# Performance work log

Hardware: AMD Instinct MI355X
Metric: run time of the kernel (lower is better)

The kernel has to match this reference:

```python
import jax, jax.numpy as jnp
import numpy as np

SEQ_LEN = 4_194_304  # number of tokens
INPUT_BITS = 16      # bits per token, MSB first


def setup_inputs() -> dict:
    key = jax.random.key(0)
    # bits in {0,1}; float32 carrier (values exact, matches uint8 bit semantics)
    tokens = jax.random.randint(key, (SEQ_LEN, INPUT_BITS), 0, 2).astype(jnp.float32)
    return {"tokens": tokens}


def reference(tokens):
    # tokens: [seq_len, input_bits], MSB first, entries in {0,1}
    bits = tokens.shape[1]
    # _bits_to_int: val = val*2 + b  ==  dot with [2^(bits-1), ..., 2, 1]
    pow2 = jnp.exp2(jnp.arange(bits - 1, -1, -1, dtype=jnp.float32))  # [bits]
    values = tokens @ pow2  # [seq_len], exact for bits <= 24
    # stable ascending sort == Python list.sort on (value, original_index)
    order = jnp.argsort(values, stable=True)  # [seq_len]
    return tokens[order]  # gather rows by rank
```

## Files before the change

### kernel.cpp

```cpp
#include <hip/hip_runtime.h>
#include <stdint.h>

static constexpr uint32_t SEQN = 4194304u;
static constexpr uint32_t BINS = 65536u;
static constexpr uint32_t QWORDS = BINS / 4u;
static constexpr uint32_t NBLK = 256u;
static constexpr uint32_t NTHR = 1024u;
static constexpr uint32_t ROWS_PER_BLK = SEQN / NBLK;

__global__ __launch_bounds__(NTHR) void k_hist_lds(const float4* __restrict__ in4,
                                                   uint32_t* __restrict__ partial,
                                                   uint32_t* __restrict__ blkTot) {
  __shared__ __align__(16) uint32_t h[QWORDS];
  uint32_t tid = threadIdx.x, blk = blockIdx.x;
  if (blk == 0u && tid < 64u) blkTot[tid] = 0u;
  uint4* hv = (uint4*)h;
  for (uint32_t i = tid; i < QWORDS / 4u; i += NTHR) hv[i] = make_uint4(0u, 0u, 0u, 0u);
  __syncthreads();
  uint32_t q = tid & 3u;
  uint32_t shift = 12u - (q << 2);
  bool leader = (q == 0u);
  const float4* base = in4 + (size_t)blk * (ROWS_PER_BLK * 4u);
#pragma unroll
  for (uint32_t b = 0; b < 8u; ++b) {
    float4 v[8];
#pragma unroll
    for (uint32_t u = 0; u < 8u; ++u)
      v[u] = base[(size_t)(b * 8u + u) * NTHR + tid];
#pragma unroll
    for (uint32_t u = 0; u < 8u; ++u) {
      float nf = ((v[u].x * 2.0f + v[u].y) * 2.0f + v[u].z) * 2.0f + v[u].w;
      uint32_t part = ((uint32_t)nf) << shift;
      uint32_t s1 = part + (uint32_t)__builtin_amdgcn_mov_dpp((int)part, 0xB1, 0xF, 0xF, true);
      uint32_t key = s1 + (uint32_t)__builtin_amdgcn_mov_dpp((int)s1, 0x4E, 0xF, 0xF, true);
      if (leader) atomicAdd(&h[key >> 2], 1u << ((key & 3u) << 3));
    }
  }
  __syncthreads();
  uint4* dst = (uint4*)(partial + (size_t)blk * QWORDS);
  for (uint32_t i = tid; i < QWORDS / 4u; i += NTHR) dst[i] = hv[i];
}

__global__ __launch_bounds__(256) void k_reduceD(const uint32_t* __restrict__ partial,
                                                 uint32_t* __restrict__ hist,
                                                 uint32_t* __restrict__ blkTot) {
  __shared__ uint2 acc[4][64];
  uint32_t tid = threadIdx.x, b = blockIdx.x;
  uint32_t wl = tid & 63u, g = tid >> 6;
  uint32_t w = b * 64u + wl;
  uint32_t e = 0u, o = 0u;
  uint32_t p0 = g * 64u;
#pragma unroll 8
  for (uint32_t p = p0; p < p0 + 64u; ++p) {
    uint32_t v = partial[(size_t)p * QWORDS + w];
    e += v & 0x00FF00FFu;
    o += (v >> 8) & 0x00FF00FFu;
  }
  acc[g][wl] = make_uint2(e, o);
  __syncthreads();
  if (g == 0u) {
    uint2 a1 = acc[1][wl], a2 = acc[2][wl], a3 = acc[3][wl];
    e += a1.x + a2.x + a3.x;
    o += a1.y + a2.y + a3.y;
    uint32_t c0 = e & 0xFFFFu, c2 = e >> 16, c1 = o & 0xFFFFu, c3 = o >> 16;
    ((uint4*)hist)[w] = make_uint4(c0, c1, c2, c3);
    uint32_t ssum = c0 + c1 + c2 + c3;
    for (int d = 1; d < 64; d <<= 1) ssum += __shfl_xor(ssum, d, 64);
    if (wl == 0u) atomicAdd(&blkTot[b >> 2], ssum);
  }
}

__global__ __launch_bounds__(256) void k_zero(uint32_t* __restrict__ hist,
                                              uint32_t* __restrict__ blkTot) {
  uint32_t i = blockIdx.x * 256u + threadIdx.x;
  if (i < BINS) hist[i] = 0u;
  if (i < 64u) blkTot[i] = 0u;
}

__global__ __launch_bounds__(256) void k_hist(const float4* __restrict__ in4,
                                              uint32_t* __restrict__ hist) {
  uint32_t r = blockIdx.x * 256u + threadIdx.x;
  if (r >= SEQN) return;
  uint32_t key = 0u;
#pragma unroll
  for (uint32_t qq = 0; qq < 4u; ++qq) {
    float4 v = in4[(size_t)r * 4u + qq];
    uint32_t nib = ((uint32_t)v.x << 3) | ((uint32_t)v.y << 2) |
                   ((uint32_t)v.z << 1) | (uint32_t)v.w;
    key = (key << 4) | nib;
  }
  atomicAdd(&hist[key], 1u);
}

__global__ __launch_bounds__(256) void k_scan1(const uint32_t* __restrict__ hist,
                                               uint32_t* __restrict__ blkTot) {
  uint32_t tid = threadIdx.x, blk = blockIdx.x;
  uint32_t b0 = blk * 1024u + tid * 4u;
  uint32_t s = hist[b0] + hist[b0 + 1] + hist[b0 + 2] + hist[b0 + 3];
  for (int d = 1; d < 64; d <<= 1) s += __shfl_xor(s, d, 64);
  __shared__ uint32_t wt[4];
  if ((tid & 63u) == 0u) wt[tid >> 6] = s;
  __syncthreads();
  if (tid == 0u) blkTot[blk] = wt[0] + wt[1] + wt[2] + wt[3];
}

__global__ __launch_bounds__(256) void k_scanB(const uint32_t* __restrict__ hist,
                                               const uint32_t* __restrict__ blkTot,
                                               uint32_t* __restrict__ offs) {
  __shared__ uint32_t s_base;
  __shared__ uint32_t wt[4];
  uint32_t tid = threadIdx.x, blk = blockIdx.x;
  if (tid < 64u) {
    uint32_t v = blkTot[tid];
    uint32_t incl = v;
    for (int d = 1; d < 64; d <<= 1) {
      uint32_t n = __shfl_up(incl, d, 64);
      if (tid >= (uint32_t)d) incl += n;
    }
    if (tid == blk) s_base = incl - v;
  }
  __syncthreads();
  uint32_t lane = tid & 63u, wid = tid >> 6;
  uint32_t b0 = blk * 1024u + tid * 4u;
  uint4 c = ((const uint4*)hist)[b0 >> 2];
  uint32_t s = c.x + c.y + c.z + c.w;
  uint32_t incl = s;
  for (int d = 1; d < 64; d <<= 1) {
    uint32_t n = __shfl_up(incl, d, 64);
    if (lane >= (uint32_t)d) incl += n;
  }
  if (lane == 63u) wt[wid] = incl;
  __syncthreads();
  uint32_t wbase = 0u;
  for (uint32_t w = 0; w < wid; ++w) wbase += wt[w];
  uint32_t base = s_base + wbase + (incl - s);
  ((uint4*)offs)[b0 >> 2] = make_uint4(base, base + c.x, base + c.x + c.y,
                                       base + c.x + c.y + c.z);
}

__global__ __launch_bounds__(256) void k_write(const uint32_t* __restrict__ hist,
                                               const uint32_t* __restrict__ offs,
                                               float4* __restrict__ out4) {
  __shared__ uint32_t s_off[32], s_cnt[32];
  uint32_t tid = threadIdx.x, blk = blockIdx.x;
  if (tid < 32u) {
    uint32_t k = blk * 32u + tid;
    s_off[tid] = offs[k];
    s_cnt[tid] = hist[k];
  }
  __syncthreads();
  uint32_t lane = tid & 63u, wid = tid >> 6;
  uint32_t q = lane & 3u;
  for (uint32_t kk = 0; kk < 8u; ++kk) {
    uint32_t ki = wid * 8u + kk;
    uint32_t k = blk * 32u + ki;
    uint32_t off = s_off[ki], cnt = s_cnt[ki];
    float4 pat;
    pat.x = (float)((k >> (15u - (q * 4u + 0u))) & 1u);
    pat.y = (float)((k >> (15u - (q * 4u + 1u))) & 1u);
    pat.z = (float)((k >> (15u - (q * 4u + 2u))) & 1u);
    pat.w = (float)((k >> (15u - (q * 4u + 3u))) & 1u);
    size_t base = (size_t)off * 4u;
    uint32_t tot = cnt * 4u;
    for (uint32_t j = lane; j < tot; j += 64u) out4[base + j] = pat;
  }
}

extern "C" void kernel_launch(void* const* d_in, const int* in_sizes, int n_in,
                              void* d_out, int out_size, void* d_ws, size_t ws_size,
                              hipStream_t stream) {
  const float4* in4 = (const float4*)d_in[0];
  float4* out4 = (float4*)d_out;
  uint32_t* hist = (uint32_t*)d_ws;
  uint32_t* offs = hist + BINS;
  uint32_t* blkTot = offs + BINS;
  uint32_t* partial = blkTot + 1024u;

  size_t need = ((size_t)2 * BINS + 1024u + (size_t)NBLK * QWORDS) * 4u;
  if (ws_size >= need) {
    k_hist_lds<<<NBLK, NTHR, 0, stream>>>(in4, partial, blkTot);
    k_reduceD<<<256, 256, 0, stream>>>(partial, hist, blkTot);
  } else {
    k_zero<<<BINS / 256, 256, 0, stream>>>(hist, blkTot);
    k_hist<<<SEQN / 256, 256, 0, stream>>>(in4, hist);
    k_scan1<<<64, 256, 0, stream>>>(hist, blkTot);
  }
  k_scanB<<<64, 256, 0, stream>>>(hist, blkTot, offs);
  k_write<<<BINS / 32, 256, 0, stream>>>(hist, offs, out4);
}
```

Baseline: 134.2 us.

## Write output by row slabs using binary search over bin offsets

The output writer now maps threads to output rows instead of histogram bins. Each block binary-searches the exclusive prefix offsets to find the key for each of its 2048 rows, stages the keys in LDS, then writes fully coalesced float4 runs. This removes the load imbalance and partial-wavefront stores that came from variable bin counts. The cost is 16 dependent global loads per row for the search, though those reads mostly hit cache.

```diff
diff --git a/kernel.cpp b/kernel.cpp
--- a/kernel.cpp
+++ b/kernel.cpp
@@ -138,31 +138,36 @@
                                        base + c.x + c.y + c.z);
 }
 
-__global__ __launch_bounds__(256) void k_write(const uint32_t* __restrict__ hist,
-                                               const uint32_t* __restrict__ offs,
-                                               float4* __restrict__ out4) {
-  __shared__ uint32_t s_off[32], s_cnt[32];
+__global__ __launch_bounds__(256) void k_write_slab(const uint32_t* __restrict__ offs,
+                                                    float4* __restrict__ out4) {
+  __shared__ uint16_t rowkey[2048];
   uint32_t tid = threadIdx.x, blk = blockIdx.x;
-  if (tid < 32u) {
-    uint32_t k = blk * 32u + tid;
-    s_off[tid] = offs[k];
-    s_cnt[tid] = hist[k];
+  uint32_t row0 = blk * 2048u;
+  uint32_t lo = 0u;
+#pragma unroll
+  for (uint32_t i = 0; i < 8u; ++i) {
+    uint32_t r = row0 + i * 256u + tid;
+    uint32_t hi = 65536u;
+    while (hi - lo > 1u) {
+      uint32_t mid = (lo + hi) >> 1;
+      if (offs[mid] <= r) lo = mid; else hi = mid;
+    }
+    rowkey[i * 256u + tid] = (uint16_t)lo;
   }
   __syncthreads();
-  uint32_t lane = tid & 63u, wid = tid >> 6;
-  uint32_t q = lane & 3u;
-  for (uint32_t kk = 0; kk < 8u; ++kk) {
-    uint32_t ki = wid * 8u + kk;
-    uint32_t k = blk * 32u + ki;
-    uint32_t off = s_off[ki], cnt = s_cnt[ki];
+  size_t qbase = (size_t)blk * 8192u;
+#pragma unroll 4
+  for (uint32_t i = 0; i < 32u; ++i) {
+    uint32_t g = i * 256u + tid;
+    uint32_t key = rowkey[g >> 2];
+    uint32_t qi = g & 3u;
+    uint32_t nib = (key >> (12u - (qi << 2))) & 15u;
     float4 pat;
-    pat.x = (float)((k >> (15u - (q * 4u + 0u))) & 1u);
-    pat.y = (float)((k >> (15u - (q * 4u + 1u))) & 1u);
-    pat.z = (float)((k >> (15u - (q * 4u + 2u))) & 1u);
-    pat.w = (float)((k >> (15u - (q * 4u + 3u))) & 1u);
-    size_t base = (size_t)off * 4u;
-    uint32_t tot = cnt * 4u;
-    for (uint32_t j = lane; j < tot; j += 64u) out4[base + j] = pat;
+    pat.x = (float)((nib >> 3) & 1u);
+    pat.y = (float)((nib >> 2) & 1u);
+    pat.z = (float)((nib >> 1) & 1u);
+    pat.w = (float)(nib & 1u);
+    out4[qbase + g] = pat;
   }
 }
 
@@ -186,5 +191,5 @@
     k_scan1<<<64, 256, 0, stream>>>(hist, blkTot);
   }
   k_scanB<<<64, 256, 0, stream>>>(hist, blkTot, offs);
-  k_write<<<BINS / 32, 256, 0, stream>>>(hist, offs, out4);
+  k_write_slab<<<SEQN / 2048, 256, 0, stream>>>(offs, out4);
 }
```

Result: slower. 149.5 us (+11.5%).
